# Performance work log

Hardware: AMD Instinct MI355X
Metric: run time of the kernel (lower is better)

The kernel has to match this reference:

```python
import jax, jax.numpy as jnp
import numpy as np

E, R, D, DFF, L, H, B, S = 10000, 200, 64, 256, 2, 8, 8, 1024
N = B * S            # total quadruples
QPQ = 3              # qualifiers per quadruple
Q = N * QPQ


def setup_inputs() -> dict:
    key = jax.random.key(0)
    ks = jax.random.split(key, 32)
    def nrm(k, shape, scale=0.05):
        return jax.random.normal(k, shape, dtype=jnp.float32) * scale
    return {
        # int index arrays (pre-tokenized entity/relation names)
        'head_idx': jax.random.randint(ks[0], (N,), 0, E, dtype=jnp.int32),
        'rel_idx': jax.random.randint(ks[1], (N,), 0, R, dtype=jnp.int32),
        'tail_idx': jax.random.randint(ks[2], (N,), 0, E, dtype=jnp.int32),
        'qual_type_idx': jax.random.randint(ks[3], (Q,), 0, R, dtype=jnp.int32),
        'qual_value_idx': jax.random.randint(ks[4], (Q,), 0, E, dtype=jnp.int32),
        'qual_seg': jnp.repeat(jnp.arange(N, dtype=jnp.int32), QPQ),  # sorted, every quad has >=1 qualifier
        # tokenizer params
        'entity_emb': nrm(ks[5], (E, D)),
        'rel_emb': nrm(ks[6], (R, D)),
        'mlp_W1': nrm(ks[7], (2 * D, D)),
        'mlp_b1': jnp.zeros((D,), jnp.float32),
        'mlp_W2': nrm(ks[8], (D, D)),
        'mlp_b2': jnp.zeros((D,), jnp.float32),
        'attn_w': nrm(ks[9], (D,)),  # AttentionAggregator scoring vector
        'proj_W': nrm(ks[10], (4 * D, D)),
        'proj_b': jnp.zeros((D,), jnp.float32),
        # transformer encoder params (post-norm, relu FFN), stacked over L layers
        'Wqkv': nrm(ks[11], (L, D, 3 * D)),
        'bqkv': jnp.zeros((L, 3 * D), jnp.float32),
        'Wo': nrm(ks[12], (L, D, D)),
        'bo': jnp.zeros((L, D), jnp.float32),
        'ln1_s': jnp.ones((L, D), jnp.float32),
        'ln1_b': jnp.zeros((L, D), jnp.float32),
        'Wff1': nrm(ks[13], (L, D, DFF)),
        'bff1': jnp.zeros((L, DFF), jnp.float32),
        'Wff2': nrm(ks[14], (L, DFF, D)),
        'bff2': jnp.zeros((L, D), jnp.float32),
        'ln2_s': jnp.ones((L, D), jnp.float32),
        'ln2_b': jnp.zeros((L, D), jnp.float32),
    }


def _ln(x, s, b):
    m = x.mean(-1, keepdims=True)
    v = ((x - m) ** 2).mean(-1, keepdims=True)
    return (x - m) / jnp.sqrt(v + 1e-5) * s + b


def _forward(head_idx, rel_idx, tail_idx, qual_type_idx, qual_value_idx, qual_seg,
             entity_emb, rel_emb, mlp_W1, mlp_b1, mlp_W2, mlp_b2, attn_w,
             proj_W, proj_b, Wqkv, bqkv, Wo, bo, ln1_s, ln1_b,
             Wff1, bff1, Wff2, bff2, ln2_s, ln2_b):
    # ---- qualifier MLP over all qualifiers at once: [Q, 2D] -> [Q, D]
    qx = jnp.concatenate([rel_emb[qual_type_idx], entity_emb[qual_value_idx]], axis=-1)
    pq = jax.nn.relu(qx @ mlp_W1 + mlp_b1) @ mlp_W2 + mlp_b2  # [Q, D]
    # ---- ragged per-quadruple attention pooling as a segment softmax
    s = pq @ attn_w                                            # [Q]
    m = jax.ops.segment_max(s, qual_seg, num_segments=N)       # [N]
    e = jnp.exp(s - m[qual_seg])
    den = jax.ops.segment_sum(e, qual_seg, num_segments=N)
    w = e / den[qual_seg]
    agg = jax.ops.segment_sum(pq * w[:, None], qual_seg, num_segments=N)  # [N, D]
    # ---- token assembly: gather + concat + linear projection
    tok_in = jnp.concatenate(
        [entity_emb[head_idx], rel_emb[rel_idx], entity_emb[tail_idx], agg], axis=-1)  # [N, 4D]
    x = (tok_in @ proj_W + proj_b).reshape(B, S, D)
    # ---- transformer encoder (post-norm, relu, no dropout)
    dh = D // H
    scale = 1.0 / np.sqrt(dh).astype(np.float32)
    for i in range(L):
        qkv = x @ Wqkv[i] + bqkv[i]
        q, k, v = jnp.split(qkv, 3, axis=-1)
        q = q.reshape(B, S, H, dh)
        k = k.reshape(B, S, H, dh)
        v = v.reshape(B, S, H, dh)
        att = jax.nn.softmax(jnp.einsum('bqhd,bkhd->bhqk', q, k) * scale, axis=-1)
        o = jnp.einsum('bhqk,bkhd->bqhd', att, v).reshape(B, S, D) @ Wo[i] + bo[i]
        x = _ln(x + o, ln1_s[i], ln1_b[i])
        f = jax.nn.relu(x @ Wff1[i] + bff1[i]) @ Wff2[i] + bff2[i]
        x = _ln(x + f, ln2_s[i], ln2_b[i])
    return x  # [B, S, D]


def reference(head_idx, rel_idx, tail_idx, qual_type_idx, qual_value_idx, qual_seg,
              entity_emb, rel_emb, mlp_W1, mlp_b1, mlp_W2, mlp_b2, attn_w,
              proj_W, proj_b, Wqkv, bqkv, Wo, bo, ln1_s, ln1_b,
              Wff1, bff1, Wff2, bff2, ln2_s, ln2_b):
    return _forward(head_idx, rel_idx, tail_idx, qual_type_idx, qual_value_idx, qual_seg,
                    entity_emb, rel_emb, mlp_W1, mlp_b1, mlp_W2, mlp_b2, attn_w,
                    proj_W, proj_b, Wqkv, bqkv, Wo, bo, ln1_s, ln1_b,
                    Wff1, bff1, Wff2, bff2, ln2_s, ln2_b)
```

## Files before the change

kernel.cpp:

```cpp
#include <hip/hip_runtime.h>
#include <hip/hip_bf16.h>
#include <hip/hip_fp16.h>

constexpr int E = 10000, R = 200, D = 64, DFF = 256, L = 2, H = 8, B = 8, S = 1024;
constexpr int N = B * S;
constexpr int QPQ = 3;
constexpr int QQ = N * QPQ;
constexpr int DH = D / H;

typedef _Float16 h2 __attribute__((ext_vector_type(2)));
typedef __fp16 fp16x2 __attribute__((ext_vector_type(2)));
typedef _Float16 f16x4 __attribute__((ext_vector_type(4)));
typedef _Float16 f16x8 __attribute__((ext_vector_type(8)));
typedef float f32x4 __attribute__((ext_vector_type(4)));
union F4H { float4 f4; h2 h[4]; f16x8 v8; };

__device__ __forceinline__ h2 pack2(float a, float b) {
#if __has_builtin(__builtin_amdgcn_cvt_pkrtz)
    fp16x2 r = __builtin_amdgcn_cvt_pkrtz(a, b);
    return __builtin_bit_cast(h2, r);
#else
    h2 r; r.x = (_Float16)a; r.y = (_Float16)b; return r;
#endif
}
__device__ __forceinline__ f32x4 mfma16(f16x8 a, f16x8 b, f32x4 c) {
    return __builtin_amdgcn_mfma_f32_16x16x32_f16(a, b, c, 0, 0, 0);
}
__device__ __forceinline__ f32x4 mfma16k16(f16x4 a, f16x4 b, f32x4 c) {
    return __builtin_amdgcn_mfma_f32_16x16x16f16(a, b, c, 0, 0, 0);
}

__device__ __forceinline__ float wsum64(float v) {
#pragma unroll
    for (int off = 32; off; off >>= 1) v += __shfl_xor(v, off, 64);
    return v;
}

constexpr int OFFB_WO   = 0;
constexpr int OFFB_WF1  = 4096;
constexpr int OFFB_WF2  = 20480;
constexpr int OFFB_WQKV = 36864;
constexpr int BFRAG_PER_LAYER = 49152;
constexpr int BF_THREADS = 12288;

constexpr int OFFB2_W1   = 0;
constexpr int OFFB2_W2   = 8192;
constexpr int OFFB2_PROJ = 12288;
constexpr int BF2_THREADS = 3584;
constexpr int PREP_THREADS = BF_THREADS + BF2_THREADS;

__global__ void prep_all(const float* __restrict__ Wo, const float* __restrict__ Wf1,
                         const float* __restrict__ Wf2, const float* __restrict__ Wqkv,
                         const float* __restrict__ W1, const float* __restrict__ W2,
                         const float* __restrict__ projW,
                         _Float16* __restrict__ out, _Float16* __restrict__ out2) {
    const int t0 = blockIdx.x * 256 + threadIdx.x;
    if (t0 < BF_THREADS) {
        const int t = t0;
        const int l = t / 6144;
        int u = t - l * 6144;
        const int lane = u & 63;
        const int ar = lane & 15, ag = lane >> 4;
        const float* src; int Nn, t_n, s, off, chunk;
        if (u < 512) {
            chunk = u >> 6; t_n = chunk >> 1; s = chunk & 1;
            src = Wo + l * 4096; Nn = 64; off = OFFB_WO;
        } else if (u < 2560) { u -= 512;
            chunk = u >> 6; t_n = chunk >> 1; s = chunk & 1;
            src = Wf1 + l * 16384; Nn = 256; off = OFFB_WF1;
        } else if (u < 4608) { u -= 2560;
            chunk = u >> 6; t_n = chunk >> 3; s = chunk & 7;
            src = Wf2 + l * 16384; Nn = 64; off = OFFB_WF2;
        } else { u -= 4608;
            chunk = u >> 6; t_n = chunk >> 1; s = chunk & 1;
            src = Wqkv + l * 12288; Nn = 192; off = OFFB_WQKV;
        }
        _Float16* dst = out + (size_t)l * BFRAG_PER_LAYER + off + ((size_t)chunk * 64 + lane) * 8;
        const int col = t_n * 16 + ar;
#pragma unroll
        for (int i = 0; i < 8; i++) {
            const int k = s * 32 + ag * 8 + i;
            dst[i] = (_Float16)src[k * Nn + col];
        }
        return;
    }
    const int t = t0 - BF_THREADS;
    if (t >= BF2_THREADS) return;
    const int lane = t & 63;
    const int ar = lane & 15, ag = lane >> 4;
    const float* src; int t_n, s, off, chunk;
    if (t < 1024) {
        chunk = t >> 6; t_n = chunk >> 2; s = chunk & 3;
        src = W1; off = OFFB2_W1;
    } else if (t < 1536) {
        const int u = t - 1024;
        chunk = u >> 6; t_n = chunk >> 1; s = chunk & 1;
        src = W2; off = OFFB2_W2;
    } else {
        const int u = t - 1536;
        chunk = u >> 6; t_n = chunk >> 3; s = chunk & 7;
        src = projW; off = OFFB2_PROJ;
    }
    _Float16* dst = out2 + off + ((size_t)chunk * 64 + lane) * 8;
    const int col = t_n * 16 + ar;
#pragma unroll
    for (int i = 0; i < 8; i++) {
        const int k = s * 32 + ag * 8 + i;
        dst[i] = (_Float16)src[k * 64 + col];
    }
}

__global__ __launch_bounds__(256, 2)
void front_kernel(const int* __restrict__ head, const int* __restrict__ rel,
                  const int* __restrict__ tail,
                  const int* __restrict__ qt, const int* __restrict__ qv,
                  const float* __restrict__ ent_emb, const float* __restrict__ rel_emb,
                  const _Float16* __restrict__ W1B, const float* __restrict__ b1,
                  const _Float16* __restrict__ W2B, const float* __restrict__ b2,
                  const float* __restrict__ attn_w,
                  const _Float16* __restrict__ projB, const float* __restrict__ projb,
                  const _Float16* __restrict__ qkv0B, const float* __restrict__ bqkv0,
                  float* __restrict__ x, _Float16* __restrict__ qkvh) {
    const int tid = threadIdx.x, wave = tid >> 6, lane = tid & 63;
    const int n0 = blockIdx.x * 16;
    const int q0 = n0 * 3;
    const int ar = lane & 15, ag = lane >> 4;

    __shared__ _Float16 qx[48][136];
    __shared__ _Float16 hs[48][72];
    __shared__ _Float16 ps[48][72];
    __shared__ _Float16 tok[16][264];
    __shared__ _Float16 act[16][72];
    __shared__ int qts[48], qvs[48], hd[16], rl[16], tl[16];
    __shared__ float s_lds[48];
    __shared__ float wsf[16][3];

    if (tid < 48) qts[tid] = qt[q0 + tid];
    else if (tid < 96) qvs[tid - 48] = qv[q0 + tid - 48];
    else if (tid < 112) hd[tid - 96] = head[n0 + tid - 96];
    else if (tid < 128) rl[tid - 112] = rel[n0 + tid - 112];
    else if (tid < 144) tl[tid - 128] = tail[n0 + tid - 128];
    __syncthreads();

#pragma unroll
    for (int i = 0; i < 24; i++) {
        const int f = tid + i * 256;
        const int row = f >> 7, col = f & 127;
        const float v = (col < 64) ? rel_emb[qts[row] * D + col]
                                   : ent_emb[(size_t)qvs[row] * D + (col - 64)];
        qx[row][col] = (_Float16)v;
    }
    __syncthreads();

    {
        const int col = wave * 16 + ar;
        const float bb = b1[col];
#pragma unroll
        for (int rt = 0; rt < 3; rt++) {
            f32x4 c = {0.f, 0.f, 0.f, 0.f};
#pragma unroll
            for (int s = 0; s < 4; s++) {
                const f16x8 a = *(const f16x8*)&qx[rt * 16 + ar][s * 32 + ag * 8];
                const f16x8 b = *(const f16x8*)&W1B[((size_t)(wave * 4 + s) * 64 + lane) * 8];
                c = mfma16(a, b, c);
            }
#pragma unroll
            for (int j = 0; j < 4; j++)
                hs[rt * 16 + ag * 4 + j][col] = (_Float16)fmaxf(c[j] + bb, 0.f);
        }
    }
    __syncthreads();

    {
        const int col = wave * 16 + ar;
        const float bb = b2[col];
#pragma unroll
        for (int rt = 0; rt < 3; rt++) {
            f32x4 c = {0.f, 0.f, 0.f, 0.f};
#pragma unroll
            for (int s = 0; s < 2; s++) {
                const f16x8 a = *(const f16x8*)&hs[rt * 16 + ar][s * 32 + ag * 8];
                const f16x8 b = *(const f16x8*)&W2B[((size_t)(wave * 2 + s) * 64 + lane) * 8];
                c = mfma16(a, b, c);
            }
#pragma unroll
            for (int j = 0; j < 4; j++)
                ps[rt * 16 + ag * 4 + j][col] = (_Float16)(c[j] + bb);
        }
    }
    __syncthreads();

    {
        const float aw = attn_w[lane];
#pragma unroll
        for (int r = 0; r < 12; r++) {
            const int row = wave * 12 + r;
            const float sv = wsum64((float)ps[row][lane] * aw);
            if (lane == 0) s_lds[row] = sv;
        }
    }
    __syncthreads();
    if (tid < 16) {
        const float s0 = s_lds[tid * 3 + 0], s1 = s_lds[tid * 3 + 1], s2 = s_lds[tid * 3 + 2];
        const float mm = fmaxf(s0, fmaxf(s1, s2));
        const float e0 = __expf(s0 - mm), e1 = __expf(s1 - mm), e2 = __expf(s2 - mm);
        const float rd = 1.f / (e0 + e1 + e2);
        wsf[tid][0] = e0 * rd; wsf[tid][1] = e1 * rd; wsf[tid][2] = e2 * rd;
    }
    __syncthreads();

#pragma unroll
    for (int i = 0; i < 16; i++) {
        const int f = tid + i * 256;
        const int row = f >> 8, col = f & 255;
        float v;
        if (col < 64)       v = ent_emb[(size_t)hd[row] * D + col];
        else if (col < 128) v = rel_emb[rl[row] * D + (col - 64)];
        else if (col < 192) v = ent_emb[(size_t)tl[row] * D + (col - 128)];
        else {
            const int c = col - 192;
            v = wsf[row][0] * (float)ps[row * 3 + 0][c] +
                wsf[row][1] * (float)ps[row * 3 + 1][c] +
                wsf[row][2] * (float)ps[row * 3 + 2][c];
        }
        tok[row][col] = (_Float16)v;
    }
    __syncthreads();

    {
        f32x4 c = {0.f, 0.f, 0.f, 0.f};
#pragma unroll
        for (int st = 0; st < 8; st++) {
            const f16x8 a = *(const f16x8*)&tok[ar][st * 32 + ag * 8];
            const f16x8 b = *(const f16x8*)&projB[((size_t)(wave * 8 + st) * 64 + lane) * 8];
            c = mfma16(a, b, c);
        }
        const int col = wave * 16 + ar;
        const float bb = projb[col];
#pragma unroll
        for (int j = 0; j < 4; j++) {
            const int row = ag * 4 + j;
            const float xv = c[j] + bb;
            x[(size_t)(n0 + row) * D + col] = xv;
            act[row][col] = (_Float16)xv;
        }
    }
    __syncthreads();

    {
        const f16x8 a0 = *(const f16x8*)&act[ar][ag * 8];
        const f16x8 a1 = *(const f16x8*)&act[ar][32 + ag * 8];
#pragma unroll
        for (int tt = 0; tt < 3; tt++) {
            const int tn = wave * 3 + tt;
            const f16x8 b0 = *(const f16x8*)&qkv0B[((size_t)(tn * 2 + 0) * 64 + lane) * 8];
            const f16x8 b1 = *(const f16x8*)&qkv0B[((size_t)(tn * 2 + 1) * 64 + lane) * 8];
            f32x4 c = {0.f, 0.f, 0.f, 0.f};
            c = mfma16(a0, b0, c);
            c = mfma16(a1, b1, c);
            const int col = tn * 16 + ar;
            const float bb = bqkv0[col];
#pragma unroll
            for (int j = 0; j < 4; j++)
                qkvh[(size_t)(n0 + ag * 4 + j) * 192 + col] = (_Float16)(c[j] + bb);
        }
    }
}

__global__ __launch_bounds__(256, 4)
void attn_kernel(const _Float16* __restrict__ qkvh, _Float16* __restrict__ out) {
    const int bid = blockIdx.x;
    const int qc = bid & 15;
    const int h = (bid >> 4) & 7;
    const int b = bid >> 7;
    const int tid = threadIdx.x, wave = tid >> 6, lane = tid & 63;
    const int ar = lane & 15, ag = lane >> 4;

    constexpr int VP = 1032;
    __shared__ _Float16 Kl[S][8];
    __shared__ _Float16 Vt[8][VP];

    const _Float16* base = qkvh + (size_t)b * S * 192;
    const _Float16 sch = (_Float16)0.3535533905932738f;
    const h2 sc2 = {sch, sch};
    for (int it = 0; it < 4; it++) {
        const int key = it * 256 + tid;
        F4H u; u.f4 = *(const float4*)(base + (size_t)key * 192 + 64 + h * 8);
#pragma unroll
        for (int i = 0; i < 4; i++) u.h[i] = u.h[i] * sc2;
        *(float4*)&Kl[key][0] = u.f4;
        F4H v; v.f4 = *(const float4*)(base + (size_t)key * 192 + 128 + h * 8);
        const _Float16* vp = (const _Float16*)&v;
#pragma unroll
        for (int d = 0; d < 8; d++) Vt[d][key] = vp[d];
    }
    __syncthreads();

    const int q0 = qc * 64 + wave * 16;
    f16x4 qf = {};
    if (ag < 2)
        qf = *(const f16x4*)(base + (size_t)(q0 + ar) * 192 + h * 8 + ag * 4);

    f32x4 oacc = {0.f, 0.f, 0.f, 0.f};
    float lsum = 0.f;
    const int vd = ar & 7;
    for (int t = 0; t < 64; t++) {
        const int k16 = t * 16;
        const f16x4 kf = *(const f16x4*)&Kl[k16 + ar][(ag & 1) * 4];
        f32x4 s4 = {0.f, 0.f, 0.f, 0.f};
        s4 = mfma16k16(kf, qf, s4);
        const float p0 = __expf(s4[0]), p1 = __expf(s4[1]);
        const float p2 = __expf(s4[2]), p3 = __expf(s4[3]);
        lsum += (p0 + p1) + (p2 + p3);
        union { h2 q[2]; f16x4 v; } pu;
        pu.q[0] = pack2(p0, p1); pu.q[1] = pack2(p2, p3);
        const f16x4 vf = *(const f16x4*)&Vt[vd][k16 + ag * 4];
        oacc = mfma16k16(pu.v, vf, oacc);
    }
    lsum += __shfl_xor(lsum, 16, 64);
    lsum += __shfl_xor(lsum, 32, 64);
    _Float16* op = out + ((size_t)(b * S + q0)) * 64 + h * 8;
#pragma unroll
    for (int j = 0; j < 4; j++) {
        const float lq = __shfl(lsum, 4 * ag + j, 64);
        if (ar < 8)
            op[(size_t)(4 * ag + j) * 64 + ar] = (_Float16)(oacc[j] / lq);
    }
}

__global__ __launch_bounds__(256, 2)
void fused_tail_kernel(float* __restrict__ x, const _Float16* __restrict__ att16,
                       const _Float16* __restrict__ WoB, const float* __restrict__ bo,
                       const float* __restrict__ ln1s, const float* __restrict__ ln1b,
                       const _Float16* __restrict__ Wf1B, const float* __restrict__ bf1,
                       const _Float16* __restrict__ Wf2B, const float* __restrict__ bf2,
                       const float* __restrict__ ln2s, const float* __restrict__ ln2b,
                       const _Float16* __restrict__ WqB, const float* __restrict__ bqkvN,
                       _Float16* __restrict__ qkvh, int do_qkv) {
    const int tid = threadIdx.x, wave = tid >> 6, lane = tid & 63;
    const int n0 = blockIdx.x * 16;
    const int ar = lane & 15, ag = lane >> 4;

    __shared__ _Float16 act[16][72];
    __shared__ float    xs0[16][76];
    __shared__ _Float16 xs1[16][72];
    __shared__ _Float16 f1s[16][264];

    if (tid < 128) {
        const int r = tid >> 3, c8 = tid & 7;
        *(f16x8*)&act[r][c8 * 8] = *(const f16x8*)&att16[((size_t)(n0 + r)) * 64 + c8 * 8];
    }
    __syncthreads();

    {
        const f16x8 a0 = *(const f16x8*)&act[ar][ag * 8];
        const f16x8 a1 = *(const f16x8*)&act[ar][32 + ag * 8];
        const f16x8 b0 = *(const f16x8*)&WoB[((size_t)(wave * 2 + 0) * 64 + lane) * 8];
        const f16x8 b1 = *(const f16x8*)&WoB[((size_t)(wave * 2 + 1) * 64 + lane) * 8];
        f32x4 c = {0.f, 0.f, 0.f, 0.f};
        c = mfma16(a0, b0, c);
        c = mfma16(a1, b1, c);
        const int col = wave * 16 + ar;
        const float bb = bo[col];
#pragma unroll
        for (int j = 0; j < 4; j++) {
            const int row = ag * 4 + j;
            xs0[row][col] = x[(size_t)(n0 + row) * D + col] + c[j] + bb;
        }
    }
    __syncthreads();

    {
        const float l1s_ = ln1s[lane], l1b_ = ln1b[lane];
#pragma unroll
        for (int r = 0; r < 4; r++) {
            const int row = wave * 4 + r;
            const float t = xs0[row][lane];
            const float mean = wsum64(t) * (1.f / 64.f);
            const float dv = t - mean;
            const float var = wsum64(dv * dv) * (1.f / 64.f);
            xs1[row][lane] = (_Float16)(dv * rsqrtf(var + 1e-5f) * l1s_ + l1b_);
        }
    }
    __syncthreads();

    {
        const f16x8 a0 = *(const f16x8*)&xs1[ar][ag * 8];
        const f16x8 a1 = *(const f16x8*)&xs1[ar][32 + ag * 8];
#pragma unroll
        for (int tt = 0; tt < 4; tt++) {
            const int tn = wave * 4 + tt;
            const f16x8 b0 = *(const f16x8*)&Wf1B[((size_t)(tn * 2 + 0) * 64 + lane) * 8];
            const f16x8 b1 = *(const f16x8*)&Wf1B[((size_t)(tn * 2 + 1) * 64 + lane) * 8];
            f32x4 c = {0.f, 0.f, 0.f, 0.f};
            c = mfma16(a0, b0, c);
            c = mfma16(a1, b1, c);
            const int col = tn * 16 + ar;
            const float bb = bf1[col];
#pragma unroll
            for (int j = 0; j < 4; j++)
                f1s[ag * 4 + j][col] = (_Float16)fmaxf(c[j] + bb, 0.f);
        }
    }
    __syncthreads();

    {
        f32x4 c = {0.f, 0.f, 0.f, 0.f};
#pragma unroll
        for (int s = 0; s < 8; s++) {
            const f16x8 a = *(const f16x8*)&f1s[ar][s * 32 + ag * 8];
            const f16x8 b = *(const f16x8*)&Wf2B[((size_t)(wave * 8 + s) * 64 + lane) * 8];
            c = mfma16(a, b, c);
        }
        const int col = wave * 16 + ar;
        const float bb = bf2[col];
#pragma unroll
        for (int j = 0; j < 4; j++) {
            const int row = ag * 4 + j;
            xs0[row][col] = (float)xs1[row][col] + c[j] + bb;
        }
    }
    __syncthreads();

    {
        const float l2s_ = ln2s[lane], l2b_ = ln2b[lane];
#pragma unroll
        for (int r = 0; r < 4; r++) {
            const int row = wave * 4 + r;
            const float t = xs0[row][lane];
            const float mean = wsum64(t) * (1.f / 64.f);
            const float dv = t - mean;
            const float var = wsum64(dv * dv) * (1.f / 64.f);
            const float xo = dv * rsqrtf(var + 1e-5f) * l2s_ + l2b_;
            x[(size_t)(n0 + row) * D + lane] = xo;
            act[row][lane] = (_Float16)xo;
        }
    }
    if (!do_qkv) return;
    __syncthreads();

    {
        const f16x8 a0 = *(const f16x8*)&act[ar][ag * 8];
        const f16x8 a1 = *(const f16x8*)&act[ar][32 + ag * 8];
#pragma unroll
        for (int tt = 0; tt < 3; tt++) {
            const int tn = wave * 3 + tt;
            const f16x8 b0 = *(const f16x8*)&WqB[((size_t)(tn * 2 + 0) * 64 + lane) * 8];
            const f16x8 b1 = *(const f16x8*)&WqB[((size_t)(tn * 2 + 1) * 64 + lane) * 8];
            f32x4 c = {0.f, 0.f, 0.f, 0.f};
            c = mfma16(a0, b0, c);
            c = mfma16(a1, b1, c);
            const int col = tn * 16 + ar;
            const float bb = bqkvN[col];
#pragma unroll
            for (int j = 0; j < 4; j++)
                qkvh[(size_t)(n0 + ag * 4 + j) * 192 + col] = (_Float16)(c[j] + bb);
        }
    }
}

extern "C" void kernel_launch(void* const* d_in, const int* in_sizes, int n_in,
                              void* d_out, int out_size, void* d_ws, size_t ws_size,
                              hipStream_t stream) {
    const int*   head_idx  = (const int*)d_in[0];
    const int*   rel_idx   = (const int*)d_in[1];
    const int*   tail_idx  = (const int*)d_in[2];
    const int*   qual_type = (const int*)d_in[3];
    const int*   qual_val  = (const int*)d_in[4];
    const float* ent_emb = (const float*)d_in[6];
    const float* rel_emb = (const float*)d_in[7];
    const float* mlp_W1  = (const float*)d_in[8];
    const float* mlp_b1  = (const float*)d_in[9];
    const float* mlp_W2  = (const float*)d_in[10];
    const float* mlp_b2  = (const float*)d_in[11];
    const float* attn_w  = (const float*)d_in[12];
    const float* proj_W  = (const float*)d_in[13];
    const float* proj_b  = (const float*)d_in[14];
    const float* Wqkv    = (const float*)d_in[15];
    const float* bqkv    = (const float*)d_in[16];
    const float* Wo      = (const float*)d_in[17];
    const float* bo      = (const float*)d_in[18];
    const float* ln1_s   = (const float*)d_in[19];
    const float* ln1_b   = (const float*)d_in[20];
    const float* Wff1    = (const float*)d_in[21];
    const float* bff1    = (const float*)d_in[22];
    const float* Wff2    = (const float*)d_in[23];
    const float* bff2    = (const float*)d_in[24];
    const float* ln2_s   = (const float*)d_in[25];
    const float* ln2_b   = (const float*)d_in[26];

    float* x = (float*)d_out;

    _Float16* att16 = (_Float16*)d_ws;
    _Float16* qkvh  = att16 + (size_t)N * 64;
    _Float16* wbf   = qkvh + (size_t)N * 192;
    _Float16* wbf2  = wbf + (size_t)2 * BFRAG_PER_LAYER;

    prep_all<<<(PREP_THREADS + 255) / 256, 256, 0, stream>>>(
        Wo, Wff1, Wff2, Wqkv, mlp_W1, mlp_W2, proj_W, wbf, wbf2);
    front_kernel<<<N / 16, 256, 0, stream>>>(head_idx, rel_idx, tail_idx,
                                             qual_type, qual_val, ent_emb, rel_emb,
                                             wbf2 + OFFB2_W1, mlp_b1,
                                             wbf2 + OFFB2_W2, mlp_b2, attn_w,
                                             wbf2 + OFFB2_PROJ, proj_b,
                                             wbf + OFFB_WQKV, bqkv, x, qkvh);
    for (int l = 0; l < L; l++) {
        attn_kernel<<<B * H * (S / 64), 256, 0, stream>>>(qkvh, att16);
        const int nl = (l + 1 < L) ? (l + 1) : 0;
        const _Float16* wb = wbf + (size_t)l * BFRAG_PER_LAYER;
        fused_tail_kernel<<<N / 16, 256, 0, stream>>>(
            x, att16,
            wb + OFFB_WO, bo + l * D, ln1_s + l * D, ln1_b + l * D,
            wb + OFFB_WF1, bff1 + l * DFF,
            wb + OFFB_WF2, bff2 + l * D,
            ln2_s + l * D, ln2_b + l * D,
            wbf + (size_t)nl * BFRAG_PER_LAYER + OFFB_WQKV, bqkv + nl * 3 * D,
            qkvh, (l + 1 < L) ? 1 : 0);
    }
}
```

Baseline: 81.59 us.

## Prefetch MFMA weight fragments into registers ahead of barriers and split attention accumulators

Across the tokenizer and FFN kernels, weight fragments for each upcoming MFMA stage are now loaded into registers before the preceding barrier, so global-load latency overlaps the current stage's work. The attention kernel issues the Q load before staging K/V and alternates between two independent accumulators to shorten the MFMA dependency chain. The FFN kernel reads the attention output straight from global memory, skipping the shared-memory staging and its barrier, and reuses the xs1 buffer in place of act. This raises register pressure and may lower occupancy.

Result: faster. 79.09 us (median of 2 runs) (-3.1%).

```diff
diff --git a/kernel.cpp b/kernel.cpp
--- a/kernel.cpp
+++ b/kernel.cpp
@@ -140,6 +140,13 @@
     else if (tid < 112) hd[tid - 96] = head[n0 + tid - 96];
     else if (tid < 128) rl[tid - 112] = rel[n0 + tid - 112];
     else if (tid < 144) tl[tid - 128] = tail[n0 + tid - 128];
+
+    f16x8 w1f[4];
+#pragma unroll
+    for (int s = 0; s < 4; s++)
+        w1f[s] = *(const f16x8*)&W1B[((size_t)(wave * 4 + s) * 64 + lane) * 8];
+    const int colw = wave * 16 + ar;
+    const float bb1 = b1[colw], bb2 = b2[colw];
     __syncthreads();
 
 #pragma unroll
@@ -150,42 +157,44 @@
                                    : ent_emb[(size_t)qvs[row] * D + (col - 64)];
         qx[row][col] = (_Float16)v;
     }
-    __syncthreads();
-
-    {
-        const int col = wave * 16 + ar;
-        const float bb = b1[col];
+    f16x8 w2f[2];
+#pragma unroll
+    for (int s = 0; s < 2; s++)
+        w2f[s] = *(const f16x8*)&W2B[((size_t)(wave * 2 + s) * 64 + lane) * 8];
+    __syncthreads();
+
+    {
 #pragma unroll
         for (int rt = 0; rt < 3; rt++) {
             f32x4 c = {0.f, 0.f, 0.f, 0.f};
 #pragma unroll
             for (int s = 0; s < 4; s++) {
                 const f16x8 a = *(const f16x8*)&qx[rt * 16 + ar][s * 32 + ag * 8];
-                const f16x8 b = *(const f16x8*)&W1B[((size_t)(wave * 4 + s) * 64 + lane) * 8];
-                c = mfma16(a, b, c);
+                c = mfma16(a, w1f[s], c);
             }
 #pragma unroll
             for (int j = 0; j < 4; j++)
-                hs[rt * 16 + ag * 4 + j][col] = (_Float16)fmaxf(c[j] + bb, 0.f);
-        }
-    }
-    __syncthreads();
-
-    {
-        const int col = wave * 16 + ar;
-        const float bb = b2[col];
+                hs[rt * 16 + ag * 4 + j][colw] = (_Float16)fmaxf(c[j] + bb1, 0.f);
+        }
+    }
+    f16x8 pjf[8];
+#pragma unroll
+    for (int st = 0; st < 8; st++)
+        pjf[st] = *(const f16x8*)&projB[((size_t)(wave * 8 + st) * 64 + lane) * 8];
+    __syncthreads();
+
+    {
 #pragma unroll
         for (int rt = 0; rt < 3; rt++) {
             f32x4 c = {0.f, 0.f, 0.f, 0.f};
 #pragma unroll
             for (int s = 0; s < 2; s++) {
                 const f16x8 a = *(const f16x8*)&hs[rt * 16 + ar][s * 32 + ag * 8];
-                const f16x8 b = *(const f16x8*)&W2B[((size_t)(wave * 2 + s) * 64 + lane) * 8];
-                c = mfma16(a, b, c);
+                c = mfma16(a, w2f[s], c);
             }
 #pragma unroll
             for (int j = 0; j < 4; j++)
-                ps[rt * 16 + ag * 4 + j][col] = (_Float16)(c[j] + bb);
+                ps[rt * 16 + ag * 4 + j][colw] = (_Float16)(c[j] + bb2);
         }
     }
     __syncthreads();
@@ -225,6 +234,13 @@
         }
         tok[row][col] = (_Float16)v;
     }
+    f16x8 qvf[6];
+#pragma unroll
+    for (int tt = 0; tt < 3; tt++) {
+        const int tn = wave * 3 + tt;
+        qvf[2 * tt]     = *(const f16x8*)&qkv0B[((size_t)(tn * 2 + 0) * 64 + lane) * 8];
+        qvf[2 * tt + 1] = *(const f16x8*)&qkv0B[((size_t)(tn * 2 + 1) * 64 + lane) * 8];
+    }
     __syncthreads();
 
     {
@@ -232,17 +248,15 @@
 #pragma unroll
         for (int st = 0; st < 8; st++) {
             const f16x8 a = *(const f16x8*)&tok[ar][st * 32 + ag * 8];
-            const f16x8 b = *(const f16x8*)&projB[((size_t)(wave * 8 + st) * 64 + lane) * 8];
-            c = mfma16(a, b, c);
-        }
-        const int col = wave * 16 + ar;
-        const float bb = projb[col];
+            c = mfma16(a, pjf[st], c);
+        }
+        const float bb = projb[colw];
 #pragma unroll
         for (int j = 0; j < 4; j++) {
             const int row = ag * 4 + j;
             const float xv = c[j] + bb;
-            x[(size_t)(n0 + row) * D + col] = xv;
-            act[row][col] = (_Float16)xv;
+            x[(size_t)(n0 + row) * D + colw] = xv;
+            act[row][colw] = (_Float16)xv;
         }
     }
     __syncthreads();
@@ -253,11 +267,9 @@
 #pragma unroll
         for (int tt = 0; tt < 3; tt++) {
             const int tn = wave * 3 + tt;
-            const f16x8 b0 = *(const f16x8*)&qkv0B[((size_t)(tn * 2 + 0) * 64 + lane) * 8];
-            const f16x8 b1 = *(const f16x8*)&qkv0B[((size_t)(tn * 2 + 1) * 64 + lane) * 8];
             f32x4 c = {0.f, 0.f, 0.f, 0.f};
-            c = mfma16(a0, b0, c);
-            c = mfma16(a1, b1, c);
+            c = mfma16(a0, qvf[2 * tt], c);
+            c = mfma16(a1, qvf[2 * tt + 1], c);
             const int col = tn * 16 + ar;
             const float bb = bqkv0[col];
 #pragma unroll
@@ -281,6 +293,12 @@
     __shared__ _Float16 Vt[8][VP];
 
     const _Float16* base = qkvh + (size_t)b * S * 192;
+
+    const int q0 = qc * 64 + wave * 16;
+    f16x4 qf = {};
+    if (ag < 2)
+        qf = *(const f16x4*)(base + (size_t)(q0 + ar) * 192 + h * 8 + ag * 4);
+
     const _Float16 sch = (_Float16)0.3535533905932738f;
     const h2 sc2 = {sch, sch};
     for (int it = 0; it < 4; it++) {
@@ -296,27 +314,34 @@
     }
     __syncthreads();
 
-    const int q0 = qc * 64 + wave * 16;
-    f16x4 qf = {};
-    if (ag < 2)
-        qf = *(const f16x4*)(base + (size_t)(q0 + ar) * 192 + h * 8 + ag * 4);
-
-    f32x4 oacc = {0.f, 0.f, 0.f, 0.f};
-    float lsum = 0.f;
+    f32x4 oacc0 = {0.f, 0.f, 0.f, 0.f}, oacc1 = {0.f, 0.f, 0.f, 0.f};
+    float lsum0 = 0.f, lsum1 = 0.f;
     const int vd = ar & 7;
-    for (int t = 0; t < 64; t++) {
-        const int k16 = t * 16;
-        const f16x4 kf = *(const f16x4*)&Kl[k16 + ar][(ag & 1) * 4];
-        f32x4 s4 = {0.f, 0.f, 0.f, 0.f};
-        s4 = mfma16k16(kf, qf, s4);
-        const float p0 = __expf(s4[0]), p1 = __expf(s4[1]);
-        const float p2 = __expf(s4[2]), p3 = __expf(s4[3]);
-        lsum += (p0 + p1) + (p2 + p3);
-        union { h2 q[2]; f16x4 v; } pu;
-        pu.q[0] = pack2(p0, p1); pu.q[1] = pack2(p2, p3);
-        const f16x4 vf = *(const f16x4*)&Vt[vd][k16 + ag * 4];
-        oacc = mfma16k16(pu.v, vf, oacc);
-    }
+    for (int t = 0; t < 64; t += 2) {
+#pragma unroll
+        for (int uu = 0; uu < 2; uu++) {
+            const int k16 = (t + uu) * 16;
+            const f16x4 kf = *(const f16x4*)&Kl[k16 + ar][(ag & 1) * 4];
+            f32x4 s4 = {0.f, 0.f, 0.f, 0.f};
+            s4 = mfma16k16(kf, qf, s4);
+            const float p0 = __expf(s4[0]), p1 = __expf(s4[1]);
+            const float p2 = __expf(s4[2]), p3 = __expf(s4[3]);
+            union { h2 q[2]; f16x4 v; } pu;
+            pu.q[0] = pack2(p0, p1); pu.q[1] = pack2(p2, p3);
+            const f16x4 vf = *(const f16x4*)&Vt[vd][k16 + ag * 4];
+            if (uu == 0) {
+                lsum0 += (p0 + p1) + (p2 + p3);
+                oacc0 = mfma16k16(pu.v, vf, oacc0);
+            } else {
+                lsum1 += (p0 + p1) + (p2 + p3);
+                oacc1 = mfma16k16(pu.v, vf, oacc1);
+            }
+        }
+    }
+    float lsum = lsum0 + lsum1;
+    f32x4 oacc;
+#pragma unroll
+    for (int j = 0; j < 4; j++) oacc[j] = oacc0[j] + oacc1[j];
     lsum += __shfl_xor(lsum, 16, 64);
     lsum += __shfl_xor(lsum, 32, 64);
     _Float16* op = out + ((size_t)(b * S + q0)) * 64 + h * 8;
@@ -340,33 +365,35 @@
     const int tid = threadIdx.x, wave = tid >> 6, lane = tid & 63;
     const int n0 = blockIdx.x * 16;
     const int ar = lane & 15, ag = lane >> 4;
-
-    __shared__ _Float16 act[16][72];
+    const int colw = wave * 16 + ar;
+
     __shared__ float    xs0[16][76];
     __shared__ _Float16 xs1[16][72];
     __shared__ _Float16 f1s[16][264];
 
-    if (tid < 128) {
-        const int r = tid >> 3, c8 = tid & 7;
-        *(f16x8*)&act[r][c8 * 8] = *(const f16x8*)&att16[((size_t)(n0 + r)) * 64 + c8 * 8];
-    }
-    __syncthreads();
-
-    {
-        const f16x8 a0 = *(const f16x8*)&act[ar][ag * 8];
-        const f16x8 a1 = *(const f16x8*)&act[ar][32 + ag * 8];
+    {
+        const f16x8 a0 = *(const f16x8*)&att16[((size_t)(n0 + ar)) * 64 + ag * 8];
+        const f16x8 a1 = *(const f16x8*)&att16[((size_t)(n0 + ar)) * 64 + 32 + ag * 8];
         const f16x8 b0 = *(const f16x8*)&WoB[((size_t)(wave * 2 + 0) * 64 + lane) * 8];
         const f16x8 b1 = *(const f16x8*)&WoB[((size_t)(wave * 2 + 1) * 64 + lane) * 8];
+        float res[4];
+#pragma unroll
+        for (int j = 0; j < 4; j++)
+            res[j] = x[(size_t)(n0 + ag * 4 + j) * D + colw];
         f32x4 c = {0.f, 0.f, 0.f, 0.f};
         c = mfma16(a0, b0, c);
         c = mfma16(a1, b1, c);
-        const int col = wave * 16 + ar;
-        const float bb = bo[col];
-#pragma unroll
-        for (int j = 0; j < 4; j++) {
-            const int row = ag * 4 + j;
-            xs0[row][col] = x[(size_t)(n0 + row) * D + col] + c[j] + bb;
-        }
+        const float bb = bo[colw];
+#pragma unroll
+        for (int j = 0; j < 4; j++)
+            xs0[ag * 4 + j][colw] = res[j] + c[j] + bb;
+    }
+    f16x8 w1f[8];
+#pragma unroll
+    for (int tt = 0; tt < 4; tt++) {
+        const int tn = wave * 4 + tt;
+        w1f[2 * tt]     = *(const f16x8*)&Wf1B[((size_t)(tn * 2 + 0) * 64 + lane) * 8];
+        w1f[2 * tt + 1] = *(const f16x8*)&Wf1B[((size_t)(tn * 2 + 1) * 64 + lane) * 8];
     }
     __syncthreads();
 
@@ -382,6 +409,10 @@
             xs1[row][lane] = (_Float16)(dv * rsqrtf(var + 1e-5f) * l1s_ + l1b_);
         }
     }
+    f16x8 w2f[8];
+#pragma unroll
+    for (int s = 0; s < 8; s++)
+        w2f[s] = *(const f16x8*)&Wf2B[((size_t)(wave * 8 + s) * 64 + lane) * 8];
     __syncthreads();
 
     {
@@ -390,11 +421,9 @@
 #pragma unroll
         for (int tt = 0; tt < 4; tt++) {
             const int tn = wave * 4 + tt;
-            const f16x8 b0 = *(const f16x8*)&Wf1B[((size_t)(tn * 2 + 0) * 64 + lane) * 8];
-            const f16x8 b1 = *(const f16x8*)&Wf1B[((size_t)(tn * 2 + 1) * 64 + lane) * 8];
             f32x4 c = {0.f, 0.f, 0.f, 0.f};
-            c = mfma16(a0, b0, c);
-            c = mfma16(a1, b1, c);
+            c = mfma16(a0, w1f[2 * tt], c);
+            c = mfma16(a1, w1f[2 * tt + 1], c);
             const int col = tn * 16 + ar;
             const float bb = bf1[col];
 #pragma unroll
@@ -402,6 +431,15 @@
                 f1s[ag * 4 + j][col] = (_Float16)fmaxf(c[j] + bb, 0.f);
         }
     }
+    f16x8 qvf[6];
+    if (do_qkv) {
+#pragma unroll
+        for (int tt = 0; tt < 3; tt++) {
+            const int tn = wave * 3 + tt;
+            qvf[2 * tt]     = *(const f16x8*)&WqB[((size_t)(tn * 2 + 0) * 64 + lane) * 8];
+            qvf[2 * tt + 1] = *(const f16x8*)&WqB[((size_t)(tn * 2 + 1) * 64 + lane) * 8];
+        }
+    }
     __syncthreads();
 
     {
@@ -409,15 +447,13 @@
 #pragma unroll
         for (int s = 0; s < 8; s++) {
             const f16x8 a = *(const f16x8*)&f1s[ar][s * 32 + ag * 8];
-            const f16x8 b = *(const f16x8*)&Wf2B[((size_t)(wave * 8 + s) * 64 + lane) * 8];
-            c = mfma16(a, b, c);
-        }
-        const int col = wave * 16 + ar;
-        const float bb = bf2[col];
+            c = mfma16(a, w2f[s], c);
+        }
+        const float bb = bf2[colw];
 #pragma unroll
         for (int j = 0; j < 4; j++) {
             const int row = ag * 4 + j;
-            xs0[row][col] = (float)xs1[row][col] + c[j] + bb;
+            xs0[row][colw] = (float)xs1[row][colw] + c[j] + bb;
         }
     }
     __syncthreads();
@@ -433,23 +469,21 @@
             const float var = wsum64(dv * dv) * (1.f / 64.f);
             const float xo = dv * rsqrtf(var + 1e-5f) * l2s_ + l2b_;
             x[(size_t)(n0 + row) * D + lane] = xo;
-            act[row][lane] = (_Float16)xo;
+            xs1[row][lane] = (_Float16)xo;
         }
     }
     if (!do_qkv) return;
     __syncthreads();
 
     {
-        const f16x8 a0 = *(const f16x8*)&act[ar][ag * 8];
-        const f16x8 a1 = *(const f16x8*)&act[ar][32 + ag * 8];
+        const f16x8 a0 = *(const f16x8*)&xs1[ar][ag * 8];
+        const f16x8 a1 = *(const f16x8*)&xs1[ar][32 + ag * 8];
 #pragma unroll
         for (int tt = 0; tt < 3; tt++) {
             const int tn = wave * 3 + tt;
-            const f16x8 b0 = *(const f16x8*)&WqB[((size_t)(tn * 2 + 0) * 64 + lane) * 8];
-            const f16x8 b1 = *(const f16x8*)&WqB[((size_t)(tn * 2 + 1) * 64 + lane) * 8];
             f32x4 c = {0.f, 0.f, 0.f, 0.f};
-            c = mfma16(a0, b0, c);
-            c = mfma16(a1, b1, c);
+            c = mfma16(a0, qvf[2 * tt], c);
+            c = mfma16(a1, qvf[2 * tt + 1], c);
             const int col = tn * 16 + ar;
             const float bb = bqkvN[col];
 #pragma unroll
```
